# Optimization experiments

Measured on AMD Instinct MI355X. Metric: run time of the kernel, lower is better.

## Reference

```python
import jax, jax.numpy as jnp
import numpy as np

# ---- static part graph (matches torch.nonzero row-major edge order) ----
ADJ = np.array([[0,1,0,0,0,0],
                [1,0,1,1,1,1],
                [0,1,0,0,0,0],
                [0,1,0,0,0,0],
                [0,1,0,0,0,1],
                [0,1,0,0,1,0]], dtype=np.int64)
EDGES = [(int(u), int(v)) for u, v in np.argwhere(ADJ)]  # 12 edges
P = ADJ.shape[0]                 # 6 part nodes (cls_p - 1)
PART_LIST = [[] for _ in range(P)]
for u, v in EDGES:
    PART_LIST[v].append(u)
DEG = [len(l) for l in PART_LIST]  # [1,5,1,1,2,2], sum = 12
CLS_P = P + 1
IN_DIM, HID = 256, 10
N, H, W = 4, 64, 64


def spatial_coords(h, w):
    """[8,h,w] coord features, same as generate_spatial_batch (vectorized)."""
    ws = np.arange(w, dtype=np.float32); hs = np.arange(h, dtype=np.float32)
    xmin = ws / w * 2 - 1; xmax = (ws + 1) / w * 2 - 1; xctr = (xmin + xmax) / 2
    ymin = hs / h * 2 - 1; ymax = (hs + 1) / h * 2 - 1; yctr = (ymin + ymax) / 2
    f = np.zeros((h, w, 8), np.float32)
    f[..., 0] = xmin[None, :]; f[..., 1] = ymin[:, None]
    f[..., 2] = xmax[None, :]; f[..., 3] = ymax[:, None]
    f[..., 4] = xctr[None, :]; f[..., 5] = yctr[:, None]
    f[..., 6] = 1.0 / w;       f[..., 7] = 1.0 / h
    return jnp.asarray(f.transpose(2, 0, 1))


def conv1x1(x, w, b=None):
    y = jnp.einsum('nchw,oc->nohw', x, w)
    return y if b is None else y + b[None, :, None, None]


def conv3x3(x, w):
    return jax.lax.conv_general_dilated(x, w, (1, 1), 'SAME',
                                        dimension_numbers=('NCHW', 'OIHW', 'NCHW'))


def bn(x, g, b, eps=1e-5):
    mu = x.mean((0, 2, 3), keepdims=True)
    var = ((x - mu) ** 2).mean((0, 2, 3), keepdims=True)
    return (x - mu) * jax.lax.rsqrt(var + eps) * g[None, :, None, None] + b[None, :, None, None]


def setup_inputs() -> dict:
    key = jax.random.key(0)
    ks = jax.random.split(key, 16)
    s = 0.05
    return {
        'xp':      jax.random.normal(ks[0], (N, IN_DIM, H, W), jnp.float32),
        'p_nodes': jax.random.normal(ks[1], (CLS_P, N, HID, H, W), jnp.float32),
        'p_atts':  jax.random.normal(ks[2], (CLS_P, N, 1, H, W), jnp.float32),
        'W_key':  jax.random.normal(ks[3], (64, IN_DIM + 8), jnp.float32) * s,
        'b_key':  jnp.zeros((64,), jnp.float32),
        'W_q':    jax.random.normal(ks[4], (64, IN_DIM + 8), jnp.float32) * s,
        'b_q':    jnp.zeros((64,), jnp.float32),
        'W_att':  jax.random.normal(ks[5], (sum(DEG), IN_DIM + 1), jnp.float32) * s,
        'b_att':  jnp.zeros((sum(DEG),), jnp.float32),
        'W_proj': jax.random.normal(ks[6], (HID, IN_DIM), jnp.float32) * s,
        'g_proj': jnp.ones((HID,), jnp.float32),
        'bt_proj': jnp.zeros((HID,), jnp.float32),
        'W_rel1': jax.random.normal(ks[7], (2 * HID, 2 * HID, 3, 3), jnp.float32) * s,
        'g_rel1': jnp.ones((2 * HID,), jnp.float32),
        'bt_rel1': jnp.zeros((2 * HID,), jnp.float32),
        'W_rel2': jax.random.normal(ks[8], (HID, 2 * HID), jnp.float32) * s,
        'b_rel2': jnp.zeros((HID,), jnp.float32),
        'Wg':    jax.random.normal(ks[9], (P, 2, 2 * HID), jnp.float32) * s,
        'bg':    jnp.zeros((P, 2), jnp.float32),
        'Wc':    jax.random.normal(ks[10], (P, HID, 2 * HID), jnp.float32) * s,
        'g_can': jnp.ones((P, HID), jnp.float32),
        'bt_can': jnp.zeros((P, HID), jnp.float32),
    }


def reference(xp, p_nodes, p_atts,
              W_key, b_key, W_q, b_q, W_att, b_att,
              W_proj, g_proj, bt_proj, W_rel1, g_rel1, bt_rel1, W_rel2, b_rel2,
              Wg, bg, Wc, g_can, bt_can):
    n, c, h, w = xp.shape
    L = h * w
    coord = jnp.broadcast_to(spatial_coords(h, w), (n, 8, h, w))

    # ---- Dep_Context (vectorized over the P part nodes) ----
    feat = jnp.concatenate([xp, coord], axis=1)                 # [n, 264, h, w]
    key_f = conv1x1(feat, W_key, b_key).reshape(n, 64, L)       # [n, 64, L]
    p_att = p_atts[1:]                                          # [P, n, 1, h, w]
    norm = jax.nn.softmax(p_att.reshape(P, n, L), axis=-1)      # [P, n, L]
    hu_c = jnp.einsum('ncl,pnl->pnc', xp.reshape(n, c, L), norm)       # [P, n, 256]
    co_c = jnp.einsum('ncl,pnl->pnc', coord.reshape(n, 8, L), norm)    # [P, n, 8]
    cen = jnp.concatenate([hu_c, co_c], axis=-1)                # [P, n, 264]
    q = jnp.einsum('pnf,of->pno', cen, W_q) + b_q               # [P, n, 64]
    energy = jnp.einsum('pno,nol->pnl', q, key_f)               # [P, n, L]
    attn = jax.nn.sigmoid(energy).reshape(P, n, 1, h, w)
    one_m = 1.0 - p_att
    F_dep_att = attn * one_m                                    # [P, n, 1, h, w]
    F_dep = attn * xp[None] * one_m                             # [P, n, 256, h, w]

    # ---- Contexture attention heads (per-node conv, deg_i output channels) ----
    att_logits, att_soft = [], []
    off = 0
    for i in range(P):
        d = DEG[i]
        inp = jnp.concatenate([F_dep_att[i], xp], axis=1)       # [n, 257, h, w]
        logit = conv1x1(inp, W_att[off:off + d], b_att[off:off + d])
        att_logits.append(logit)
        att_soft.append(jax.nn.softmax(logit, axis=1))
        off += d

    # ---- Dependency messages per edge ----
    def dependency(hv, hu_ctx, dep_att):
        msg = jax.nn.relu(bn(conv1x1(hu_ctx * dep_att, W_proj), g_proj, bt_proj))
        x = jnp.concatenate([msg, hv], axis=1)                  # [n, 20, h, w]
        x = jax.nn.relu(bn(conv3x3(x, W_rel1), g_rel1, bt_rel1))
        return jax.nn.sigmoid(conv1x1(x, W_rel2, b_rel2))       # [n, 10, h, w]

    msgs = [None] * P
    for u, v in EDGES:
        ch = PART_LIST[u].index(v)
        # NB: original code indexes p_node_list with the raw edge target v
        m = dependency(p_nodes[v], F_dep[u], att_soft[u][:, ch:ch + 1])
        msgs[v] = m if msgs[v] is None else msgs[v] + m

    # ---- ConvGRU node updates ----
    new_nodes = [p_nodes[0]]
    for i in range(P):
        h_cur, msg = p_nodes[i + 1], msgs[i]
        gates = conv1x1(jnp.concatenate([msg, h_cur], axis=1), Wg[i], bg[i])
        r = jax.nn.sigmoid(gates[:, 0:1]); z = jax.nn.sigmoid(gates[:, 1:2])
        cnm = conv1x1(jnp.concatenate([msg, r * h_cur], axis=1), Wc[i])
        cnm = jax.nn.leaky_relu(bn(cnm, g_can[i], bt_can[i]), 0.01)  # InPlaceABNSync default
        new_nodes.append((1.0 - z) * h_cur + z * cnm)

    xp_new = jnp.stack(new_nodes)                               # [cls_p, n, 10, h, w]
    fdep_att = jnp.concatenate(att_logits, axis=1)              # [n, 12, h, w]
    return xp_new, fdep_att
```

## Files before the change

### kernel.cpp

```cpp
#include <hip/hip_runtime.h>
#include <math.h>

#define L 4096

__constant__ int c_EV[12]   = {1,0,2,3,4,5,1,1,1,5,1,4};
__constant__ int c_INOFF[7] = {0,1,6,7,8,10,12};
__constant__ int c_INE[12]  = {1, 0,6,7,8,10, 2, 3, 4,11, 5,9};

__device__ inline float sigmf(float x){ return 1.f/(1.f+expf(-x)); }

__global__ __launch_bounds__(256) void k_softmax_norm(const float* __restrict__ p_atts,
                                                      float* __restrict__ norm,
                                                      const float* __restrict__ W_rel1,
                                                      float* __restrict__ wt2){
  int tid = threadIdx.x;
  if (blockIdx.x == 24){
    for (int i = tid; i < 3600; i += 256){
      int co = i % 10; int t = i / 10;
      int k = t % 9; t /= 9;
      int h = t & 1; int ci = t >> 1;
      wt2[i] = W_rel1[(((h * 10 + co) * 20) + ci) * 9 + k];
    }
    return;
  }
  int pn = blockIdx.x;
  const float* src = p_atts + (size_t)(pn + 4) * L;
  float* dst = norm + (size_t)pn * L;
  __shared__ float red[256];
  float m = -1e30f;
  for (int l = tid; l < L; l += 256) m = fmaxf(m, src[l]);
  red[tid] = m; __syncthreads();
  for (int s = 128; s; s >>= 1){ if (tid < s) red[tid] = fmaxf(red[tid], red[tid+s]); __syncthreads(); }
  m = red[0]; __syncthreads();
  float sum = 0.f;
  for (int l = tid; l < L; l += 256) sum += expf(src[l] - m);
  red[tid] = sum; __syncthreads();
  for (int s = 128; s; s >>= 1){ if (tid < s) red[tid] += red[tid+s]; __syncthreads(); }
  float inv = 1.f / red[0];
  for (int l = tid; l < L; l += 256) dst[l] = expf(src[l] - m) * inv;
}

__device__ inline float coord_feat(int cc, int l){
  int h = l >> 6, w = l & 63;
  const float s = 2.f / 64.f;
  switch (cc){
    case 0: return w * s - 1.f;
    case 1: return h * s - 1.f;
    case 2: return (w + 1) * s - 1.f;
    case 3: return (h + 1) * s - 1.f;
    case 4: return (w + 0.5f) * s - 1.f;
    case 5: return (h + 0.5f) * s - 1.f;
    default: return 1.f / 64.f;
  }
}

__global__ __launch_bounds__(256) void k_centroid(const float* __restrict__ xp,
                                                  const float* __restrict__ norm,
                                                  float* __restrict__ cen){
  int c = blockIdx.x;
  int n = blockIdx.y;
  int tid = threadIdx.x;
  float acc[6];
#pragma unroll
  for (int p = 0; p < 6; p++) acc[p] = 0.f;
  const float* nr0 = norm + (size_t)n * L;
  if (c < 256){
    const float* xr = xp + ((size_t)n * 256 + c) * L;
    for (int l = tid; l < L; l += 256){
      float xv = xr[l];
#pragma unroll
      for (int p = 0; p < 6; p++) acc[p] = fmaf(xv, nr0[(size_t)p * 4 * L + l], acc[p]);
    }
  } else {
    int cc = c - 256;
    for (int l = tid; l < L; l += 256){
      float xv = coord_feat(cc, l);
#pragma unroll
      for (int p = 0; p < 6; p++) acc[p] = fmaf(xv, nr0[(size_t)p * 4 * L + l], acc[p]);
    }
  }
#pragma unroll
  for (int p = 0; p < 6; p++){
    for (int off = 32; off; off >>= 1) acc[p] += __shfl_xor(acc[p], off, 64);
  }
  __shared__ float red[6][4];
  int wv = tid >> 6;
  if ((tid & 63) == 0){
#pragma unroll
    for (int p = 0; p < 6; p++) red[p][wv] = acc[p];
  }
  __syncthreads();
  if (tid < 6){
    float s = red[tid][0] + red[tid][1] + red[tid][2] + red[tid][3];
    cen[(size_t)(tid * 4 + n) * 264 + c] = s;
  }
}

__global__ __launch_bounds__(256) void k_qk(const float* __restrict__ cen,
                                            const float* __restrict__ W_q, const float* __restrict__ b_q,
                                            const float* __restrict__ W_key, const float* __restrict__ b_key,
                                            float* __restrict__ qk, float* __restrict__ qb){
  int pn = blockIdx.x;
  int tid = threadIdx.x;
  __shared__ float cen_s[264];
  __shared__ float qs[64];
  __shared__ float part[256];
  for (int i = tid; i < 264; i += 256) cen_s[i] = cen[(size_t)pn * 264 + i];
  __syncthreads();
  int o = tid >> 2, pr = tid & 3;
  {
    float a = 0.f;
    int f0 = pr * 66;
    for (int j = 0; j < 66; j++){ int f = f0 + j; a = fmaf(cen_s[f], W_q[o * 264 + f], a); }
    part[tid] = a;
  }
  __syncthreads();
  if (pr == 0) qs[o] = part[tid] + part[tid + 1] + part[tid + 2] + part[tid + 3] + b_q[o];
  __syncthreads();
  for (int c = tid; c < 264; c += 256){
    float a = 0.f;
    for (int oo = 0; oo < 64; oo++) a = fmaf(qs[oo], W_key[oo * 264 + c], a);
    qk[(size_t)pn * 264 + c] = a;
  }
  if (tid < 64) part[tid] = qs[tid] * b_key[tid];
  __syncthreads();
  if (tid == 0){
    float a = 0.f;
    for (int oo = 0; oo < 64; oo++) a += part[oo];
    qb[pn] = a;
  }
}

__global__ __launch_bounds__(256) void k_pixel(const float* __restrict__ xp,
                                              const float* __restrict__ p_atts,
                                              const float* __restrict__ W_att, const float* __restrict__ b_att,
                                              const float* __restrict__ W_proj,
                                              const float* __restrict__ qk, const float* __restrict__ qb,
                                              float* __restrict__ out_fdep,
                                              float* __restrict__ s_edge,
                                              float* __restrict__ proj_x){
  __shared__ float s_watt[256 * 12];
  __shared__ float s_wproj[256 * 12];
  __shared__ float s_qk[256 * 8];
  __shared__ float s_qkt[48];
  __shared__ float pacc[4][28][64];
  __shared__ float w0[12], ba[12], qbs[6];
  int n = blockIdx.y;
  int tid = threadIdx.x;
  int wv = tid >> 6, w = tid & 63;
  int l = blockIdx.x * 64 + w;
  for (int i = tid; i < 256 * 12; i += 256){ int c = i / 12, j = i % 12; s_watt[i] = W_att[j * 257 + 1 + c]; }
  for (int i = tid; i < 256 * 12; i += 256){ int c = i / 12, k = i % 12; s_wproj[i] = (k < 10) ? W_proj[k * 256 + c] : 0.f; }
  for (int i = tid; i < 256 * 8; i += 256){ int c = i >> 3, p = i & 7; s_qk[i] = (p < 6) ? qk[((size_t)(p * 4 + n)) * 264 + c] : 0.f; }
  if (tid < 48){ int p = tid >> 3, cc = tid & 7; s_qkt[tid] = qk[((size_t)(p * 4 + n)) * 264 + 256 + cc]; }
  if (tid < 12){ w0[tid] = W_att[tid * 257]; ba[tid] = b_att[tid]; }
  if (tid < 6) qbs[tid] = qb[tid * 4 + n];
  __syncthreads();

  float a[32];
#pragma unroll
  for (int f = 0; f < 32; f++) a[f] = 0.f;
  const float* xpn = xp + (size_t)n * 256 * L + l;
  int c0 = wv * 64;
#pragma unroll 2
  for (int cc = 0; cc < 64; cc++){
    int c = c0 + cc;
    float xv = xpn[(size_t)c * L];
    float4 wa0 = *(const float4*)(s_watt + c * 12);
    float4 wa1 = *(const float4*)(s_watt + c * 12 + 4);
    float4 wa2 = *(const float4*)(s_watt + c * 12 + 8);
    float4 wp0 = *(const float4*)(s_wproj + c * 12);
    float4 wp1 = *(const float4*)(s_wproj + c * 12 + 4);
    float4 wp2 = *(const float4*)(s_wproj + c * 12 + 8);
    float4 wq0 = *(const float4*)(s_qk + c * 8);
    float4 wq1 = *(const float4*)(s_qk + c * 8 + 4);
    a[0]  = fmaf(xv, wa0.x, a[0]);  a[1]  = fmaf(xv, wa0.y, a[1]);
    a[2]  = fmaf(xv, wa0.z, a[2]);  a[3]  = fmaf(xv, wa0.w, a[3]);
    a[4]  = fmaf(xv, wa1.x, a[4]);  a[5]  = fmaf(xv, wa1.y, a[5]);
    a[6]  = fmaf(xv, wa1.z, a[6]);  a[7]  = fmaf(xv, wa1.w, a[7]);
    a[8]  = fmaf(xv, wa2.x, a[8]);  a[9]  = fmaf(xv, wa2.y, a[9]);
    a[10] = fmaf(xv, wa2.z, a[10]); a[11] = fmaf(xv, wa2.w, a[11]);
    a[12] = fmaf(xv, wp0.x, a[12]); a[13] = fmaf(xv, wp0.y, a[13]);
    a[14] = fmaf(xv, wp0.z, a[14]); a[15] = fmaf(xv, wp0.w, a[15]);
    a[16] = fmaf(xv, wp1.x, a[16]); a[17] = fmaf(xv, wp1.y, a[17]);
    a[18] = fmaf(xv, wp1.z, a[18]); a[19] = fmaf(xv, wp1.w, a[19]);
    a[20] = fmaf(xv, wp2.x, a[20]); a[21] = fmaf(xv, wp2.y, a[21]);
    a[24] = fmaf(xv, wq0.x, a[24]); a[25] = fmaf(xv, wq0.y, a[25]);
    a[26] = fmaf(xv, wq0.z, a[26]); a[27] = fmaf(xv, wq0.w, a[27]);
    a[28] = fmaf(xv, wq1.x, a[28]); a[29] = fmaf(xv, wq1.y, a[29]);
  }
#pragma unroll
  for (int f = 0; f < 12; f++) pacc[wv][f][w] = a[f];
#pragma unroll
  for (int k = 0; k < 10; k++) pacc[wv][12 + k][w] = a[12 + k];
#pragma unroll
  for (int p = 0; p < 6; p++) pacc[wv][22 + p][w] = a[24 + p];
  __syncthreads();
  for (int idx = tid; idx < 28 * 64; idx += 256){
    int f = idx >> 6, ww = idx & 63;
    pacc[0][f][ww] = pacc[0][f][ww] + pacc[1][f][ww] + pacc[2][f][ww] + pacc[3][f][ww];
  }
  __syncthreads();
  if (tid < 64){
    float accA[12], accP[10], accE[6];
#pragma unroll
    for (int j = 0; j < 12; j++) accA[j] = pacc[0][j][w];
#pragma unroll
    for (int k = 0; k < 10; k++) accP[k] = pacc[0][12 + k][w];
#pragma unroll
    for (int p = 0; p < 6; p++) accE[p] = pacc[0][22 + p][w];

    float cf[8];
    { int hh = l >> 6, ww2 = l & 63; const float s = 2.f / 64.f;
      cf[0] = ww2 * s - 1.f; cf[1] = hh * s - 1.f; cf[2] = (ww2 + 1) * s - 1.f; cf[3] = (hh + 1) * s - 1.f;
      cf[4] = (ww2 + 0.5f) * s - 1.f; cf[5] = (hh + 0.5f) * s - 1.f; cf[6] = 1.f / 64.f; cf[7] = 1.f / 64.f; }
    float sat[6];
#pragma unroll
    for (int p = 0; p < 6; p++){
      float e = accE[p] + qbs[p];
#pragma unroll
      for (int cc = 0; cc < 8; cc++) e = fmaf(cf[cc], s_qkt[p * 8 + cc], e);
      float aa = sigmf(e);
      float pa = p_atts[((size_t)(p + 1) * 4 + n) * L + l];
      sat[p] = aa * (1.f - pa);
    }
    const int part_of[12] = {0,1,1,1,1,1,2,3,4,4,5,5};
    float lg[12];
#pragma unroll
    for (int j = 0; j < 12; j++){
      lg[j] = accA[j] + w0[j] * sat[part_of[j]] + ba[j];
      out_fdep[((size_t)n * 12 + j) * L + l] = lg[j];
    }
    const int gs[6] = {0,1,6,7,8,10}, gd[6] = {1,5,1,1,2,2};
    float sm[12];
#pragma unroll
    for (int g = 0; g < 6; g++){
      int s0 = gs[g], d = gd[g];
      float mx = lg[s0];
      for (int t = 1; t < d; t++) mx = fmaxf(mx, lg[s0 + t]);
      float ssum = 0.f;
      for (int t = 0; t < d; t++){ float e2 = expf(lg[s0 + t] - mx); sm[s0 + t] = e2; ssum += e2; }
      float inv = 1.f / ssum;
      for (int t = 0; t < d; t++) sm[s0 + t] *= inv;
    }
#pragma unroll
    for (int e = 0; e < 12; e++) s_edge[((size_t)e * 4 + n) * L + l] = sat[part_of[e]] * sm[e];
#pragma unroll
    for (int k = 0; k < 10; k++) proj_x[((size_t)n * 10 + k) * L + l] = accP[k];
  }
}

__global__ __launch_bounds__(256) void k_msg_stats(const float* __restrict__ proj_x,
                                                   const float* __restrict__ s_edge,
                                                   float* __restrict__ mu, float* __restrict__ istd){
  int e = blockIdx.x / 10, k = blockIdx.x % 10;
  int tid = threadIdx.x;
  float s1 = 0.f, s2 = 0.f;
  for (int idx = tid; idx < 4 * L; idx += 256){
    int n = idx >> 12, l = idx & (L - 1);
    float t = proj_x[((size_t)n * 10 + k) * L + l] * s_edge[((size_t)e * 4 + n) * L + l];
    s1 += t; s2 += t * t;
  }
  __shared__ float r1[256], r2[256];
  r1[tid] = s1; r2[tid] = s2; __syncthreads();
  for (int s = 128; s; s >>= 1){ if (tid < s){ r1[tid] += r1[tid+s]; r2[tid] += r2[tid+s]; } __syncthreads(); }
  if (tid == 0){
    float m = r1[0] / 16384.f, v = r2[0] / 16384.f - m * m;
    mu[blockIdx.x] = m; istd[blockIdx.x] = rsqrtf(v + 1e-5f);
  }
}

__global__ __launch_bounds__(256) void k_conv3(const float* __restrict__ proj_x,
                                               const float* __restrict__ s_edge,
                                               const float* __restrict__ mu, const float* __restrict__ istd,
                                               const float* __restrict__ g_proj, const float* __restrict__ bt_proj,
                                               const float* __restrict__ p_nodes,
                                               const float* __restrict__ wt2,
                                               float* __restrict__ y,
                                               float* __restrict__ ypart){
  __shared__ float red[4][20];
  int rb = blockIdx.x, n = blockIdx.y;
  int e = blockIdx.z >> 1, h = blockIdx.z & 1;
  int v = c_EV[e];
  int tid = threadIdx.x;
  int wv = tid >> 6, w = tid & 63;
  int r0 = rb * 8 + wv * 2;
  float mLm = (w == 0) ? 0.f : 1.f;
  float mRm = (w == 63) ? 0.f : 1.f;

  float scs[10], sbs[10];
#pragma unroll
  for (int k = 0; k < 10; k++){
    int ek = e * 10 + k;
    float s = istd[ek] * g_proj[k];
    scs[k] = s; sbs[k] = bt_proj[k] - mu[ek] * s;
  }
  const size_t enL = ((size_t)e * 4 + n) * L;
  const float* se = s_edge + enL;
  float se4[4];
#pragma unroll
  for (int j = 0; j < 4; j++){
    int rr = r0 - 1 + j;
    se4[j] = (rr >= 0 && rr < 64) ? se[rr * 64 + w] : 0.f;
  }

  float acc0[10], acc1[10];
#pragma unroll
  for (int co = 0; co < 10; co++){ acc0[co] = 0.f; acc1[co] = 0.f; }

  for (int ci = 0; ci < 10; ci++){
    const float* pr = proj_x + ((size_t)n * 10 + ci) * L;
    float mC[4];
#pragma unroll
    for (int j = 0; j < 4; j++){
      int rr = r0 - 1 + j;
      if (rr >= 0 && rr < 64){
        float t = pr[rr * 64 + w] * se4[j];
        mC[j] = fmaxf(fmaf(t, scs[ci], sbs[ci]), 0.f);
      } else mC[j] = 0.f;
    }
    float mL[4], mR[4];
#pragma unroll
    for (int j = 0; j < 4; j++){
      mL[j] = __shfl_up(mC[j], 1) * mLm;
      mR[j] = __shfl_down(mC[j], 1) * mRm;
    }
    const float* wp = wt2 + (ci * 2 + h) * 90;
#pragma unroll
    for (int ky = 0; ky < 3; ky++){
#pragma unroll
      for (int co = 0; co < 10; co++){
        float w0v = wp[(ky * 3 + 0) * 10 + co];
        float w1v = wp[(ky * 3 + 1) * 10 + co];
        float w2v = wp[(ky * 3 + 2) * 10 + co];
        acc0[co] = fmaf(mL[ky], w0v, fmaf(mC[ky], w1v, fmaf(mR[ky], w2v, acc0[co])));
        acc1[co] = fmaf(mL[ky + 1], w0v, fmaf(mC[ky + 1], w1v, fmaf(mR[ky + 1], w2v, acc1[co])));
      }
    }
  }
  for (int ci = 10; ci < 20; ci++){
    const float* pnp = p_nodes + (((size_t)v * 4 + n) * 10 + (ci - 10)) * L;
    float mC[4];
#pragma unroll
    for (int j = 0; j < 4; j++){
      int rr = r0 - 1 + j;
      mC[j] = (rr >= 0 && rr < 64) ? pnp[rr * 64 + w] : 0.f;
    }
    float mL[4], mR[4];
#pragma unroll
    for (int j = 0; j < 4; j++){
      mL[j] = __shfl_up(mC[j], 1) * mLm;
      mR[j] = __shfl_down(mC[j], 1) * mRm;
    }
    const float* wp = wt2 + (ci * 2 + h) * 90;
#pragma unroll
    for (int ky = 0; ky < 3; ky++){
#pragma unroll
      for (int co = 0; co < 10; co++){
        float w0v = wp[(ky * 3 + 0) * 10 + co];
        float w1v = wp[(ky * 3 + 1) * 10 + co];
        float w2v = wp[(ky * 3 + 2) * 10 + co];
        acc0[co] = fmaf(mL[ky], w0v, fmaf(mC[ky], w1v, fmaf(mR[ky], w2v, acc0[co])));
        acc1[co] = fmaf(mL[ky + 1], w0v, fmaf(mC[ky + 1], w1v, fmaf(mR[ky + 1], w2v, acc1[co])));
      }
    }
  }

  int ch0 = h * 10;
#pragma unroll
  for (int co = 0; co < 10; co++){
    size_t base = enL * 20 + ((size_t)(ch0 + co)) * L;
    y[base + r0 * 64 + w] = acc0[co];
    y[base + (r0 + 1) * 64 + w] = acc1[co];
  }

#pragma unroll
  for (int co = 0; co < 10; co++){
    float s1 = acc0[co] + acc1[co];
    float s2 = acc0[co] * acc0[co] + acc1[co] * acc1[co];
    for (int off = 32; off; off >>= 1){ s1 += __shfl_xor(s1, off, 64); s2 += __shfl_xor(s2, off, 64); }
    if (w == 0){ red[wv][2 * co] = s1; red[wv][2 * co + 1] = s2; }
  }
  __syncthreads();
  if (tid < 20){
    int co = tid >> 1, which = tid & 1;
    float s = red[0][tid] + red[1][tid] + red[2][tid] + red[3][tid];
    ypart[(((size_t)(e * 20 + ch0 + co) * 32) + n * 8 + rb) * 2 + which] = s;
  }
}

__global__ __launch_bounds__(64) void k_red(const float* __restrict__ part, int npart,
                                            float* __restrict__ mu, float* __restrict__ istd){
  int ent = blockIdx.x;
  int t = threadIdx.x;
  float s1 = 0.f, s2 = 0.f;
  if (t < npart){
    const float* p = part + ((size_t)ent * npart + t) * 2;
    s1 = p[0]; s2 = p[1];
  }
  for (int off = 32; off; off >>= 1){ s1 += __shfl_xor(s1, off, 64); s2 += __shfl_xor(s2, off, 64); }
  if (t == 0){
    float m = s1 / 16384.f, v = s2 / 16384.f - m * m;
    mu[ent] = m; istd[ent] = rsqrtf(v + 1e-5f);
  }
}

__global__ __launch_bounds__(256) void k_mout_gru(const float* __restrict__ y,
                                                  const float* __restrict__ mu_y, const float* __restrict__ istd_y,
                                                  const float* __restrict__ g_rel1, const float* __restrict__ bt_rel1,
                                                  const float* __restrict__ W_rel2, const float* __restrict__ b_rel2,
                                                  const float* __restrict__ p_nodes,
                                                  const float* __restrict__ Wg, const float* __restrict__ bg,
                                                  const float* __restrict__ Wc,
                                                  float* __restrict__ cnm, float* __restrict__ zbuf,
                                                  float* __restrict__ cpart){
  int i = blockIdx.z, n = blockIdx.y;
  int tid = threadIdx.x;
  int l = blockIdx.x * 256 + tid;
  __shared__ float w2[200], wc[200], wg[40], bgs[2];
  __shared__ float sc[5][20], sb[5][20];
  __shared__ float red[4][20];
  int ne = c_INOFF[i + 1] - c_INOFF[i];
  for (int t = tid; t < 200; t += 256){ w2[t] = W_rel2[t]; wc[t] = Wc[i * 200 + t]; }
  if (tid < 40) wg[tid] = Wg[i * 40 + tid];
  if (tid < 2) bgs[tid] = bg[i * 2 + tid];
  if (tid < ne * 20){
    int ei = tid / 20, c = tid % 20;
    int e = c_INE[c_INOFF[i] + ei];
    int ec = e * 20 + c;
    float s = istd_y[ec] * g_rel1[c];
    sc[ei][c] = s; sb[ei][c] = bt_rel1[c] - mu_y[ec] * s;
  }
  __syncthreads();
  float m[10];
#pragma unroll
  for (int k = 0; k < 10; k++) m[k] = 0.f;
  for (int ei = 0; ei < ne; ei++){
    int e = c_INE[c_INOFF[i] + ei];
    float z[20];
#pragma unroll
    for (int c = 0; c < 20; c++){
      float t = y[(((size_t)e * 4 + n) * 20 + c) * L + l];
      z[c] = fmaxf(t * sc[ei][c] + sb[ei][c], 0.f);
    }
#pragma unroll
    for (int k = 0; k < 10; k++){
      float a = b_rel2[k];
#pragma unroll
      for (int c = 0; c < 20; c++) a = fmaf(w2[k * 20 + c], z[c], a);
      m[k] += sigmf(a);
    }
  }
  float h[10];
#pragma unroll
  for (int k = 0; k < 10; k++) h[k] = p_nodes[(((size_t)(i + 1) * 4 + n) * 10 + k) * L + l];
  float g0 = bgs[0], g1 = bgs[1];
#pragma unroll
  for (int k = 0; k < 10; k++){
    g0 = fmaf(wg[k], m[k], g0); g0 = fmaf(wg[10 + k], h[k], g0);
    g1 = fmaf(wg[20 + k], m[k], g1); g1 = fmaf(wg[30 + k], h[k], g1);
  }
  float r = sigmf(g0), zz = sigmf(g1);
  zbuf[((size_t)i * 4 + n) * L + l] = zz;
  float cv[10];
#pragma unroll
  for (int k = 0; k < 10; k++){
    float a = 0.f;
#pragma unroll
    for (int c = 0; c < 10; c++){
      a = fmaf(wc[k * 20 + c], m[c], a);
      a = fmaf(wc[k * 20 + 10 + c], r * h[c], a);
    }
    cv[k] = a;
    cnm[(((size_t)i * 4 + n) * 10 + k) * L + l] = a;
  }
  int wv = tid >> 6, w = tid & 63;
#pragma unroll
  for (int k = 0; k < 10; k++){
    float s1 = cv[k], s2 = cv[k] * cv[k];
    for (int off = 32; off; off >>= 1){ s1 += __shfl_xor(s1, off, 64); s2 += __shfl_xor(s2, off, 64); }
    if (w == 0){ red[wv][2 * k] = s1; red[wv][2 * k + 1] = s2; }
  }
  __syncthreads();
  if (tid < 20){
    float s = red[0][tid] + red[1][tid] + red[2][tid] + red[3][tid];
    int k = tid >> 1, which = tid & 1;
    cpart[(((size_t)(i * 10 + k) * 64) + n * 16 + blockIdx.x) * 2 + which] = s;
  }
}

__global__ __launch_bounds__(256) void k_out(const float* __restrict__ cnm, const float* __restrict__ zbuf,
                                             const float* __restrict__ p_nodes,
                                             const float* __restrict__ mu, const float* __restrict__ istd,
                                             const float* __restrict__ g_can, const float* __restrict__ bt_can,
                                             float* __restrict__ out){
  int idx = blockIdx.x * 256 + threadIdx.x;
  const int NODE = 4 * 10 * L;
  if (idx < NODE){ out[idx] = p_nodes[idx]; return; }
  int j = idx - NODE;
  int l = j & (L - 1); int r = j >> 12;
  int k = r % 10; r /= 10; int n = r & 3; int i = r >> 2;
  int ik = i * 10 + k;
  float c = cnm[j];
  float cn = (c - mu[ik]) * istd[ik] * g_can[ik] + bt_can[ik];
  cn = cn > 0.f ? cn : 0.01f * cn;
  float z = zbuf[((size_t)i * 4 + n) * L + l];
  float h = p_nodes[idx];
  out[idx] = (1.f - z) * h + z * cn;
}

extern "C" void kernel_launch(void* const* d_in, const int* in_sizes, int n_in,
                              void* d_out, int out_size, void* d_ws, size_t ws_size,
                              hipStream_t stream){
  (void)in_sizes; (void)n_in; (void)out_size; (void)ws_size;
  const float* xp      = (const float*)d_in[0];
  const float* p_nodes = (const float*)d_in[1];
  const float* p_atts  = (const float*)d_in[2];
  const float* W_key   = (const float*)d_in[3];
  const float* b_key   = (const float*)d_in[4];
  const float* W_q     = (const float*)d_in[5];
  const float* b_q     = (const float*)d_in[6];
  const float* W_att   = (const float*)d_in[7];
  const float* b_att   = (const float*)d_in[8];
  const float* W_proj  = (const float*)d_in[9];
  const float* g_proj  = (const float*)d_in[10];
  const float* bt_proj = (const float*)d_in[11];
  const float* W_rel1  = (const float*)d_in[12];
  const float* g_rel1  = (const float*)d_in[13];
  const float* bt_rel1 = (const float*)d_in[14];
  const float* W_rel2  = (const float*)d_in[15];
  const float* b_rel2  = (const float*)d_in[16];
  const float* Wg      = (const float*)d_in[17];
  const float* bg      = (const float*)d_in[18];
  const float* Wc      = (const float*)d_in[19];
  const float* g_can   = (const float*)d_in[20];
  const float* bt_can  = (const float*)d_in[21];

  float* out      = (float*)d_out;
  float* fdep_out = out + (size_t)7 * 4 * 10 * L;

  float* w = (float*)d_ws;
  size_t off = 0;
  auto alloc = [&](size_t nf){ float* p = w + off; off += nf; return p; };
  float* norm    = alloc((size_t)6 * 4 * L);
  float* cen     = alloc(6 * 4 * 264);
  float* qk      = alloc(6 * 4 * 264);
  float* qb      = alloc(24);
  float* wt2     = alloc(3600);
  float* proj_x  = alloc((size_t)4 * 10 * L);
  float* s_edge  = alloc((size_t)12 * 4 * L);
  float* mu_msg  = alloc(120);
  float* istd_msg= alloc(120);
  float* ybuf    = alloc((size_t)12 * 4 * 20 * L);
  float* ypart   = alloc(240 * 32 * 2);
  float* cpart   = alloc(60 * 64 * 2);
  float* mu_y    = alloc(240);
  float* istd_y  = alloc(240);
  float* cnm     = alloc((size_t)6 * 4 * 10 * L);
  float* zbuf    = alloc((size_t)6 * 4 * L);
  float* mu_c    = alloc(60);
  float* istd_c  = alloc(60);

  k_softmax_norm<<<25, 256, 0, stream>>>(p_atts, norm, W_rel1, wt2);
  { dim3 g(264, 4); k_centroid<<<g, 256, 0, stream>>>(xp, norm, cen); }
  k_qk<<<24, 256, 0, stream>>>(cen, W_q, b_q, W_key, b_key, qk, qb);
  { dim3 g(64, 4); k_pixel<<<g, 256, 0, stream>>>(xp, p_atts, W_att, b_att, W_proj, qk, qb, fdep_out, s_edge, proj_x); }
  k_msg_stats<<<120, 256, 0, stream>>>(proj_x, s_edge, mu_msg, istd_msg);
  { dim3 g(8, 4, 24); k_conv3<<<g, 256, 0, stream>>>(proj_x, s_edge, mu_msg, istd_msg, g_proj, bt_proj, p_nodes, wt2, ybuf, ypart); }
  k_red<<<240, 64, 0, stream>>>(ypart, 32, mu_y, istd_y);
  { dim3 g(16, 4, 6); k_mout_gru<<<g, 256, 0, stream>>>(ybuf, mu_y, istd_y, g_rel1, bt_rel1, W_rel2, b_rel2,
                                                        p_nodes, Wg, bg, Wc, cnm, zbuf, cpart); }
  k_red<<<60, 64, 0, stream>>>(cpart, 64, mu_c, istd_c);
  k_out<<<(7 * 4 * 10 * L) / 256, 256, 0, stream>>>(cnm, zbuf, p_nodes, mu_c, istd_c, g_can, bt_can, out);
}
```

Baseline: 152.0 us.

## Fuse message BN statistics into pixel kernel and widen conv3 row tiling

Per-block partial sums and sums of squares of proj_x*s_edge are now computed inside k_pixel from values already held in LDS, and a small k_red256 kernel reduces them. This replaces the standalone k_msg_stats pass that re-read proj_x and s_edge from global memory. Separately, k_conv3 now computes 4 output rows per wave instead of 2 and halves the grid, so the 3x3 halo rows are reloaded less often, at the cost of more registers and fewer blocks in flight.

```diff
diff --git a/kernel.cpp b/kernel.cpp
--- a/kernel.cpp
+++ b/kernel.cpp
@@ -138,7 +138,8 @@
                                               const float* __restrict__ qk, const float* __restrict__ qb,
                                               float* __restrict__ out_fdep,
                                               float* __restrict__ s_edge,
-                                              float* __restrict__ proj_x){
+                                              float* __restrict__ proj_x,
+                                              float* __restrict__ mpart){
   __shared__ float s_watt[256 * 12];
   __shared__ float s_wproj[256 * 12];
   __shared__ float s_qk[256 * 8];
@@ -201,6 +202,7 @@
     pacc[0][f][ww] = pacc[0][f][ww] + pacc[1][f][ww] + pacc[2][f][ww] + pacc[3][f][ww];
   }
   __syncthreads();
+  float* se_lds = &pacc[1][0][0];
   if (tid < 64){
     float accA[12], accP[10], accE[6];
 #pragma unroll
@@ -244,29 +246,47 @@
       for (int t = 0; t < d; t++) sm[s0 + t] *= inv;
     }
 #pragma unroll
-    for (int e = 0; e < 12; e++) s_edge[((size_t)e * 4 + n) * L + l] = sat[part_of[e]] * sm[e];
+    for (int e = 0; e < 12; e++){
+      float sev = sat[part_of[e]] * sm[e];
+      s_edge[((size_t)e * 4 + n) * L + l] = sev;
+      se_lds[e * 64 + w] = sev;
+    }
 #pragma unroll
     for (int k = 0; k < 10; k++) proj_x[((size_t)n * 10 + k) * L + l] = accP[k];
   }
-}
-
-__global__ __launch_bounds__(256) void k_msg_stats(const float* __restrict__ proj_x,
-                                                   const float* __restrict__ s_edge,
-                                                   float* __restrict__ mu, float* __restrict__ istd){
-  int e = blockIdx.x / 10, k = blockIdx.x % 10;
-  int tid = threadIdx.x;
-  float s1 = 0.f, s2 = 0.f;
-  for (int idx = tid; idx < 4 * L; idx += 256){
-    int n = idx >> 12, l = idx & (L - 1);
-    float t = proj_x[((size_t)n * 10 + k) * L + l] * s_edge[((size_t)e * 4 + n) * L + l];
-    s1 += t; s2 += t * t;
-  }
-  __shared__ float r1[256], r2[256];
-  r1[tid] = s1; r2[tid] = s2; __syncthreads();
-  for (int s = 128; s; s >>= 1){ if (tid < s){ r1[tid] += r1[tid+s]; r2[tid] += r2[tid+s]; } __syncthreads(); }
-  if (tid == 0){
-    float m = r1[0] / 16384.f, v = r2[0] / 16384.f - m * m;
-    mu[blockIdx.x] = m; istd[blockIdx.x] = rsqrtf(v + 1e-5f);
+  __syncthreads();
+  {
+    int blk = n * 64 + blockIdx.x;
+#pragma unroll
+    for (int j = 0; j < 30; j++){
+      int pair = wv * 30 + j;
+      int e = pair / 10, k = pair % 10;
+      float t = se_lds[e * 64 + w] * pacc[0][12 + k][w];
+      float s1 = t, s2 = t * t;
+      for (int off = 32; off; off >>= 1){ s1 += __shfl_xor(s1, off, 64); s2 += __shfl_xor(s2, off, 64); }
+      if (w == 0){
+        mpart[((size_t)pair * 256 + blk) * 2]     = s1;
+        mpart[((size_t)pair * 256 + blk) * 2 + 1] = s2;
+      }
+    }
+  }
+}
+
+__global__ __launch_bounds__(256) void k_red256(const float* __restrict__ part,
+                                                float* __restrict__ mu, float* __restrict__ istd){
+  int ent = blockIdx.x;
+  int t = threadIdx.x;
+  const float* p = part + ((size_t)ent * 256 + t) * 2;
+  float s1 = p[0], s2 = p[1];
+  for (int off = 32; off; off >>= 1){ s1 += __shfl_xor(s1, off, 64); s2 += __shfl_xor(s2, off, 64); }
+  __shared__ float r1[4], r2[4];
+  if ((t & 63) == 0){ r1[t >> 6] = s1; r2[t >> 6] = s2; }
+  __syncthreads();
+  if (t == 0){
+    float a1 = r1[0] + r1[1] + r1[2] + r1[3];
+    float a2 = r2[0] + r2[1] + r2[2] + r2[3];
+    float m = a1 / 16384.f, v = a2 / 16384.f - m * m;
+    mu[ent] = m; istd[ent] = rsqrtf(v + 1e-5f);
   }
 }
 
@@ -284,7 +304,7 @@
   int v = c_EV[e];
   int tid = threadIdx.x;
   int wv = tid >> 6, w = tid & 63;
-  int r0 = rb * 8 + wv * 2;
+  int r0 = rb * 16 + wv * 4;
   float mLm = (w == 0) ? 0.f : 1.f;
   float mRm = (w == 63) ? 0.f : 1.f;
 
@@ -297,31 +317,32 @@
   }
   const size_t enL = ((size_t)e * 4 + n) * L;
   const float* se = s_edge + enL;
-  float se4[4];
-#pragma unroll
-  for (int j = 0; j < 4; j++){
+  float se6[6];
+#pragma unroll
+  for (int j = 0; j < 6; j++){
     int rr = r0 - 1 + j;
-    se4[j] = (rr >= 0 && rr < 64) ? se[rr * 64 + w] : 0.f;
-  }
-
-  float acc0[10], acc1[10];
-#pragma unroll
-  for (int co = 0; co < 10; co++){ acc0[co] = 0.f; acc1[co] = 0.f; }
+    se6[j] = (rr >= 0 && rr < 64) ? se[rr * 64 + w] : 0.f;
+  }
+
+  float acc[4][10];
+#pragma unroll
+  for (int j = 0; j < 4; j++)
+#pragma unroll
+    for (int co = 0; co < 10; co++) acc[j][co] = 0.f;
 
   for (int ci = 0; ci < 10; ci++){
     const float* pr = proj_x + ((size_t)n * 10 + ci) * L;
-    float mC[4];
-#pragma unroll
-    for (int j = 0; j < 4; j++){
+    float mC[6], mL[6], mR[6];
+#pragma unroll
+    for (int j = 0; j < 6; j++){
       int rr = r0 - 1 + j;
       if (rr >= 0 && rr < 64){
-        float t = pr[rr * 64 + w] * se4[j];
+        float t = pr[rr * 64 + w] * se6[j];
         mC[j] = fmaxf(fmaf(t, scs[ci], sbs[ci]), 0.f);
       } else mC[j] = 0.f;
     }
-    float mL[4], mR[4];
-#pragma unroll
-    for (int j = 0; j < 4; j++){
+#pragma unroll
+    for (int j = 0; j < 6; j++){
       mL[j] = __shfl_up(mC[j], 1) * mLm;
       mR[j] = __shfl_down(mC[j], 1) * mRm;
     }
@@ -333,22 +354,22 @@
         float w0v = wp[(ky * 3 + 0) * 10 + co];
         float w1v = wp[(ky * 3 + 1) * 10 + co];
         float w2v = wp[(ky * 3 + 2) * 10 + co];
-        acc0[co] = fmaf(mL[ky], w0v, fmaf(mC[ky], w1v, fmaf(mR[ky], w2v, acc0[co])));
-        acc1[co] = fmaf(mL[ky + 1], w0v, fmaf(mC[ky + 1], w1v, fmaf(mR[ky + 1], w2v, acc1[co])));
+#pragma unroll
+        for (int j = 0; j < 4; j++)
+          acc[j][co] = fmaf(mL[j + ky], w0v, fmaf(mC[j + ky], w1v, fmaf(mR[j + ky], w2v, acc[j][co])));
       }
     }
   }
   for (int ci = 10; ci < 20; ci++){
     const float* pnp = p_nodes + (((size_t)v * 4 + n) * 10 + (ci - 10)) * L;
-    float mC[4];
-#pragma unroll
-    for (int j = 0; j < 4; j++){
+    float mC[6], mL[6], mR[6];
+#pragma unroll
+    for (int j = 0; j < 6; j++){
       int rr = r0 - 1 + j;
       mC[j] = (rr >= 0 && rr < 64) ? pnp[rr * 64 + w] : 0.f;
     }
-    float mL[4], mR[4];
-#pragma unroll
-    for (int j = 0; j < 4; j++){
+#pragma unroll
+    for (int j = 0; j < 6; j++){
       mL[j] = __shfl_up(mC[j], 1) * mLm;
       mR[j] = __shfl_down(mC[j], 1) * mRm;
     }
@@ -360,8 +381,9 @@
         float w0v = wp[(ky * 3 + 0) * 10 + co];
         float w1v = wp[(ky * 3 + 1) * 10 + co];
         float w2v = wp[(ky * 3 + 2) * 10 + co];
-        acc0[co] = fmaf(mL[ky], w0v, fmaf(mC[ky], w1v, fmaf(mR[ky], w2v, acc0[co])));
-        acc1[co] = fmaf(mL[ky + 1], w0v, fmaf(mC[ky + 1], w1v, fmaf(mR[ky + 1], w2v, acc1[co])));
+#pragma unroll
+        for (int j = 0; j < 4; j++)
+          acc[j][co] = fmaf(mL[j + ky], w0v, fmaf(mC[j + ky], w1v, fmaf(mR[j + ky], w2v, acc[j][co])));
       }
     }
   }
@@ -370,14 +392,16 @@
 #pragma unroll
   for (int co = 0; co < 10; co++){
     size_t base = enL * 20 + ((size_t)(ch0 + co)) * L;
-    y[base + r0 * 64 + w] = acc0[co];
-    y[base + (r0 + 1) * 64 + w] = acc1[co];
+#pragma unroll
+    for (int j = 0; j < 4; j++)
+      y[base + (r0 + j) * 64 + w] = acc[j][co];
   }
 
 #pragma unroll
   for (int co = 0; co < 10; co++){
-    float s1 = acc0[co] + acc1[co];
-    float s2 = acc0[co] * acc0[co] + acc1[co] * acc1[co];
+    float s1 = acc[0][co] + acc[1][co] + acc[2][co] + acc[3][co];
+    float s2 = acc[0][co] * acc[0][co] + acc[1][co] * acc[1][co]
+             + acc[2][co] * acc[2][co] + acc[3][co] * acc[3][co];
     for (int off = 32; off; off >>= 1){ s1 += __shfl_xor(s1, off, 64); s2 += __shfl_xor(s2, off, 64); }
     if (w == 0){ red[wv][2 * co] = s1; red[wv][2 * co + 1] = s2; }
   }
@@ -385,7 +409,7 @@
   if (tid < 20){
     int co = tid >> 1, which = tid & 1;
     float s = red[0][tid] + red[1][tid] + red[2][tid] + red[3][tid];
-    ypart[(((size_t)(e * 20 + ch0 + co) * 32) + n * 8 + rb) * 2 + which] = s;
+    ypart[(((size_t)(e * 20 + ch0 + co) * 16) + n * 4 + rb) * 2 + which] = s;
   }
 }
 
@@ -549,10 +573,11 @@
   float* wt2     = alloc(3600);
   float* proj_x  = alloc((size_t)4 * 10 * L);
   float* s_edge  = alloc((size_t)12 * 4 * L);
+  float* mpart   = alloc(120 * 256 * 2);
   float* mu_msg  = alloc(120);
   float* istd_msg= alloc(120);
   float* ybuf    = alloc((size_t)12 * 4 * 20 * L);
-  float* ypart   = alloc(240 * 32 * 2);
+  float* ypart   = alloc(240 * 16 * 2);
   float* cpart   = alloc(60 * 64 * 2);
   float* mu_y    = alloc(240);
   float* istd_y  = alloc(240);
@@ -564,10 +589,10 @@
   k_softmax_norm<<<25, 256, 0, stream>>>(p_atts, norm, W_rel1, wt2);
   { dim3 g(264, 4); k_centroid<<<g, 256, 0, stream>>>(xp, norm, cen); }
   k_qk<<<24, 256, 0, stream>>>(cen, W_q, b_q, W_key, b_key, qk, qb);
-  { dim3 g(64, 4); k_pixel<<<g, 256, 0, stream>>>(xp, p_atts, W_att, b_att, W_proj, qk, qb, fdep_out, s_edge, proj_x); }
-  k_msg_stats<<<120, 256, 0, stream>>>(proj_x, s_edge, mu_msg, istd_msg);
-  { dim3 g(8, 4, 24); k_conv3<<<g, 256, 0, stream>>>(proj_x, s_edge, mu_msg, istd_msg, g_proj, bt_proj, p_nodes, wt2, ybuf, ypart); }
-  k_red<<<240, 64, 0, stream>>>(ypart, 32, mu_y, istd_y);
+  { dim3 g(64, 4); k_pixel<<<g, 256, 0, stream>>>(xp, p_atts, W_att, b_att, W_proj, qk, qb, fdep_out, s_edge, proj_x, mpart); }
+  k_red256<<<120, 256, 0, stream>>>(mpart, mu_msg, istd_msg);
+  { dim3 g(4, 4, 24); k_conv3<<<g, 256, 0, stream>>>(proj_x, s_edge, mu_msg, istd_msg, g_proj, bt_proj, p_nodes, wt2, ybuf, ypart); }
+  k_red<<<240, 64, 0, stream>>>(ypart, 16, mu_y, istd_y);
   { dim3 g(16, 4, 6); k_mout_gru<<<g, 256, 0, stream>>>(ybuf, mu_y, istd_y, g_rel1, bt_rel1, W_rel2, b_rel2,
                                                         p_nodes, Wg, bg, Wc, cnm, zbuf, cpart); }
   k_red<<<60, 64, 0, stream>>>(cpart, 64, mu_c, istd_c);
```

After: 153.1 us. Within noise of the previous version (+0.7%).
